# Performance work log

Hardware: AMD Instinct MI355X
Metric: run time of the kernel (lower is better)

Reference implementation:

```python
import jax, jax.numpy as jnp
import numpy as np

N_NODES = 100000
N_EDGES = 1600000
F_IN = 65
HIDDEN = 128
N_CLASSES = 32
NEG_SLOPE = 0.2


def _gat_conv(x0, src, dst, W, a_src, a_dst, b):
    """Single-head GAT-style conv: gather over edges, segment softmax, scatter-add."""
    h = x0 @ W                                  # [N, C]
    s = h @ a_src                                # [N]
    d = h @ a_dst                                # [N]
    e = jax.nn.leaky_relu(s[src] + d[dst], NEG_SLOPE)   # [E]
    m = jax.ops.segment_max(e, dst, num_segments=N_NODES)
    m = jnp.where(jnp.isfinite(m), m, 0.0)
    ex = jnp.exp(e - m[dst])                     # [E]
    denom = jax.ops.segment_sum(ex, dst, num_segments=N_NODES)
    alpha = ex / (denom[dst] + 1e-16)            # [E]
    out = jax.ops.segment_sum(h[src] * alpha[:, None], dst, num_segments=N_NODES)
    return out + b                               # [N, C]


def setup_inputs() -> dict:
    key = jax.random.key(0)
    ks = jax.random.split(key, 12)
    sc_in = 1.0 / np.sqrt(F_IN)
    sc_h = 1.0 / np.sqrt(HIDDEN)
    return {
        "x": jax.random.normal(ks[0], (N_NODES, F_IN), dtype=jnp.float32),
        "edge_index": jax.random.randint(ks[1], (2, N_EDGES), 0, N_NODES, dtype=jnp.int64),
        "W_mlp": jax.random.normal(ks[2], (F_IN, HIDDEN), dtype=jnp.float32) * sc_in,
        "b_mlp": jnp.zeros((HIDDEN,), dtype=jnp.float32),
        "W1": jax.random.normal(ks[3], (HIDDEN, N_CLASSES), dtype=jnp.float32) * sc_h,
        "a1_src": jax.random.normal(ks[4], (N_CLASSES,), dtype=jnp.float32) * 0.1,
        "a1_dst": jax.random.normal(ks[5], (N_CLASSES,), dtype=jnp.float32) * 0.1,
        "b1": jnp.zeros((N_CLASSES,), dtype=jnp.float32),
        "W2": jax.random.normal(ks[6], (HIDDEN, N_CLASSES), dtype=jnp.float32) * sc_h,
        "a2_src": jax.random.normal(ks[7], (N_CLASSES,), dtype=jnp.float32) * 0.1,
        "a2_dst": jax.random.normal(ks[8], (N_CLASSES,), dtype=jnp.float32) * 0.1,
        "b2": jnp.zeros((N_CLASSES,), dtype=jnp.float32),
    }


def reference(x, edge_index, W_mlp, b_mlp, W1, a1_src, a1_dst, b1, W2, a2_src, a2_dst, b2):
    src, dst = edge_index[0], edge_index[1]
    x0 = jax.nn.relu(x @ W_mlp + b_mlp)                      # [N, H]
    x1 = jax.nn.relu(_gat_conv(x0, src, dst, W1, a1_src, a1_dst, b1))  # [N, C]
    # dropout is identity in eval mode
    x2 = _gat_conv(x0, src, dst, W2, a2_src, a2_dst, b2)     # [N, C]
    x3 = jnp.max(x0, axis=-1, keepdims=True)                 # [N, 1]
    lngal_out = jnp.concatenate((x1, x2, x3), axis=-1) + x   # [N, 2C+1] == [N, F]
    return jax.nn.log_softmax(lngal_out, axis=1)
```

## Files before the change

kernel.cpp:

```cpp
#include <hip/hip_runtime.h>
#include <hip/hip_bf16.h>

#define NN 100000
#define NE 1600000
#define FIN 65
#define HID 128
#define NC 32
#define OUTC 65
#define NBUCK 391
#define CHUNKS 400
#define CH 4000
#define ESTRIDE 5120
#define NODE_BLOCKS 1563

typedef __attribute__((ext_vector_type(8))) short s8v;
typedef __attribute__((ext_vector_type(4))) float f4v;
typedef __attribute__((ext_vector_type(2))) float f2v;
#define MFMA16(a, b, c) __builtin_amdgcn_mfma_f32_16x16x32_bf16(a, b, c, 0, 0, 0)

__device__ __forceinline__ float lrelu(float v){ return v > 0.f ? v : 0.2f * v; }
__device__ __forceinline__ short f2bs(float f){
  unsigned u = __float_as_uint(f);
  u += 0x7fffu + ((u >> 16) & 1u);
  return (short)(u >> 16);
}
__device__ __forceinline__ float bfu_lo(unsigned u){ return __uint_as_float(u << 16); }
__device__ __forceinline__ float bfu_hi(unsigned u){ return __uint_as_float(u & 0xffff0000u); }
__device__ __forceinline__ unsigned char f2fp8(float f){
  int p = __builtin_amdgcn_cvt_pk_fp8_f32(f, f, 0, false);
  return (unsigned char)(p & 0xff);
}

__global__ __launch_bounds__(256) void k_prep(
    const float* __restrict__ Wmlp, const float* __restrict__ W1,
    const float* __restrict__ W2, short* __restrict__ wbg,
    int* __restrict__ bcursor)
{
  const int i = blockIdx.x * 256 + threadIdx.x;
  if (blockIdx.x == 0)
    for (int t = threadIdx.x; t < NBUCK; t += 256) bcursor[t] = 0;
  {
    const int j = i & 7, l = (i >> 3) & 63, nt = (i >> 9) & 7, t = i >> 12;
    const int k = t * 32 + ((l >> 4) << 3) + j;
    const int col = (nt << 4) + (l & 15);
    wbg[i] = f2bs(Wmlp[k * HID + col]);
  }
  {
    const int j = i & 7, l = (i >> 3) & 63, nt = (i >> 9) & 3, t = i >> 11;
    const int k = t * 32 + ((l >> 4) << 3) + j;
    const int col = (nt << 4) + (l & 15);
    wbg[8192 + i] = f2bs(col < NC ? W1[k * NC + col] : W2[k * NC + col - NC]);
  }
}

__global__ __launch_bounds__(256) void k_main(
    const float* __restrict__ x, const short* __restrict__ wbg,
    const float* __restrict__ Wmlp, const float* __restrict__ bmlp,
    const float* __restrict__ a1s, const float* __restrict__ a1d,
    const float* __restrict__ a2s, const float* __restrict__ a2d,
    const int* __restrict__ ei,
    unsigned char* __restrict__ hb8,
    float* __restrict__ sd2, float* __restrict__ dd2,
    float* __restrict__ out,
    int* __restrict__ bcursor, int* __restrict__ ebuf)
{
  __shared__ alignas(16) char smem[18944];
  const int tid = threadIdx.x;

  if (blockIdx.x >= NODE_BLOCKS) {
    const int cb = blockIdx.x - NODE_BLOCKS;
    int* lh = (int*)smem;
    int* lbase = lh + NBUCK;
    for (int i = tid; i < NBUCK; i += 256) lh[i] = 0;
    __syncthreads();
    const int4* s4 = (const int4*)ei + cb * (CH / 4);
    const int4* d4 = (const int4*)(ei + NE) + cb * (CH / 4);
    for (int i = tid; i < CH / 4; i += 256) {
      int4 v = d4[i];
      atomicAdd(&lh[v.x >> 8], 1);
      atomicAdd(&lh[v.y >> 8], 1);
      atomicAdd(&lh[v.z >> 8], 1);
      atomicAdd(&lh[v.w >> 8], 1);
    }
    __syncthreads();
    for (int i = tid; i < NBUCK; i += 256) {
      int c = lh[i];
      lbase[i] = c ? (i * ESTRIDE + atomicAdd(&bcursor[i], c)) : 0;
      lh[i] = 0;
    }
    __syncthreads();
    for (int i = tid; i < CH / 4; i += 256) {
      int4 sv = s4[i];
      int4 dv = d4[i];
      int b, r;
      b = dv.x >> 8; r = atomicAdd(&lh[b], 1); ebuf[lbase[b] + r] = (sv.x << 8) | (dv.x & 255);
      b = dv.y >> 8; r = atomicAdd(&lh[b], 1); ebuf[lbase[b] + r] = (sv.y << 8) | (dv.y & 255);
      b = dv.z >> 8; r = atomicAdd(&lh[b], 1); ebuf[lbase[b] + r] = (sv.z << 8) | (dv.z & 255);
      b = dv.w >> 8; r = atomicAdd(&lh[b], 1); ebuf[lbase[b] + r] = (sv.w << 8) | (dv.w & 255);
    }
    return;
  }

  short* x0b = (short*)smem;
  float* w64 = (float*)(smem + 17408);
  float* bmv = (float*)(smem + 17920);
  float* avv = (float*)(smem + 18432);

  const int base = blockIdx.x * 64;
  const int w = tid >> 6, lane = tid & 63;
  const int g = lane >> 4, q = lane & 15;
  const int rowA = w * 16 + q;
  const int rowD0 = w * 16 + g * 4;
  const int nodeA = base + rowA;
  const s8v* wv8 = (const s8v*)wbg;

  float xa[16];
  if (nodeA < NN) {
    const float* xr = x + (size_t)nodeA * FIN + g * 8;
    #pragma unroll
    for (int j = 0; j < 8; ++j) xa[j] = xr[j];
    #pragma unroll
    for (int j = 0; j < 8; ++j) xa[8 + j] = xr[32 + j];
  } else {
    #pragma unroll
    for (int j = 0; j < 16; ++j) xa[j] = 0.f;
  }
  float xc[4];
  #pragma unroll
  for (int r = 0; r < 4; ++r) {
    const int n2 = base + rowD0 + r;
    xc[r] = (n2 < NN) ? x[(size_t)n2 * FIN + 64] : 0.f;
  }

  if (tid < 128) { w64[tid] = Wmlp[64 * HID + tid]; bmv[tid] = bmlp[tid]; }
  else if (tid < 160) {
    const int qq = tid - 128;
    avv[qq] = a1s[qq]; avv[32 + qq] = a1d[qq]; avv[64 + qq] = a2s[qq]; avv[96 + qq] = a2d[qq];
  }
  __syncthreads();

  s8v a0, a1;
  #pragma unroll
  for (int j = 0; j < 8; ++j) { a0[j] = f2bs(xa[j]); a1[j] = f2bs(xa[8 + j]); }

  f4v acc[8];
  #pragma unroll
  for (int nt = 0; nt < 8; ++nt) acc[nt] = (f4v){0.f, 0.f, 0.f, 0.f};
  #pragma unroll
  for (int nt = 0; nt < 8; ++nt) {
    const s8v b0 = wv8[nt * 64 + lane];
    const s8v b1 = wv8[(8 + nt) * 64 + lane];
    acc[nt] = MFMA16(a0, b0, acc[nt]);
    acc[nt] = MFMA16(a1, b1, acc[nt]);
  }

  float rmax[4] = {0.f, 0.f, 0.f, 0.f};
  #pragma unroll
  for (int nt = 0; nt < 8; ++nt) {
    const int col = nt * 16 + q;
    const float wvv = w64[col], bv = bmv[col];
    #pragma unroll
    for (int r = 0; r < 4; ++r) {
      const float v = fmaxf(fmaf(xc[r], wvv, acc[nt][r]) + bv, 0.f);
      rmax[r] = fmaxf(rmax[r], v);
      x0b[(rowD0 + r) * 136 + col] = f2bs(v);
    }
  }
  #pragma unroll
  for (int off = 1; off < 16; off <<= 1)
    #pragma unroll
    for (int r = 0; r < 4; ++r) rmax[r] = fmaxf(rmax[r], __shfl_xor(rmax[r], off));
  if (q == 0) {
    #pragma unroll
    for (int r = 0; r < 4; ++r) {
      const int node = base + rowD0 + r;
      if (node < NN) out[(size_t)node * OUTC + 64] = rmax[r];
    }
  }

  s8v af[4];
  #pragma unroll
  for (int t2 = 0; t2 < 4; ++t2)
    af[t2] = *(const s8v*)&x0b[rowA * 136 + t2 * 32 + g * 8];
  f4v hacc[4];
  #pragma unroll
  for (int nt = 0; nt < 4; ++nt) hacc[nt] = (f4v){0.f, 0.f, 0.f, 0.f};
  #pragma unroll
  for (int nt = 0; nt < 4; ++nt)
    #pragma unroll
    for (int t2 = 0; t2 < 4; ++t2)
      hacc[nt] = MFMA16(af[t2], wv8[1024 + (t2 * 4 + nt) * 64 + lane], hacc[nt]);

  float s1p[4], d1p[4], s2p[4], d2p[4];
  #pragma unroll
  for (int r = 0; r < 4; ++r) {
    s1p[r] = hacc[0][r] * avv[q]        + hacc[1][r] * avv[16 + q];
    d1p[r] = hacc[0][r] * avv[32 + q]   + hacc[1][r] * avv[48 + q];
    s2p[r] = hacc[2][r] * avv[64 + q]   + hacc[3][r] * avv[80 + q];
    d2p[r] = hacc[2][r] * avv[96 + q]   + hacc[3][r] * avv[112 + q];
  }
  #pragma unroll
  for (int off = 1; off < 16; off <<= 1) {
    #pragma unroll
    for (int r = 0; r < 4; ++r) {
      s1p[r] += __shfl_xor(s1p[r], off);
      d1p[r] += __shfl_xor(d1p[r], off);
      s2p[r] += __shfl_xor(s2p[r], off);
      d2p[r] += __shfl_xor(d2p[r], off);
    }
  }
  #pragma unroll
  for (int r = 0; r < 4; ++r) {
    const int node = base + rowD0 + r;
    if (node < NN) {
      #pragma unroll
      for (int nt = 0; nt < 4; ++nt)
        hb8[(size_t)node * 64 + nt * 16 + q] = f2fp8(hacc[nt][r]);
      if (q == 0) {
        *(float2*)&sd2[(size_t)node * 2] = make_float2(s1p[r], s2p[r]);
        *(float2*)&dd2[(size_t)node * 2] = make_float2(d1p[r], d2p[r]);
      }
    }
  }
}

__global__ __launch_bounds__(256) void k_csr(const int* __restrict__ bcursor,
                                             const int* __restrict__ ebuf,
                                             int* __restrict__ rpp,
                                             int* __restrict__ csrc)
{
  __shared__ int lh[256];
  __shared__ int wsum[4];
  const int b = blockIdx.x;
  const int e0 = b * ESTRIDE;
  const int cntb = bcursor[b];
  const int t = threadIdx.x;

  lh[t] = 0;
  __syncthreads();
  for (int i = t; i < cntb; i += 256)
    atomicAdd(&lh[ebuf[e0 + i] & 255], 1);
  __syncthreads();

  const int lane = t & 63;
  const int wid = t >> 6;
  int v = lh[t];
  const int orig = v;
  for (int off = 1; off < 64; off <<= 1) {
    int tm = __shfl_up(v, off);
    if (lane >= off) v += tm;
  }
  if (lane == 63) wsum[wid] = v;
  __syncthreads();
  int add = 0;
  for (int ww = 0; ww < wid; ++ww) add += wsum[ww];
  const int ex = v + add - orig;

  const int nb0 = b << 8;
  if (nb0 + t < NN) rpp[nb0 + t] = ((e0 + ex) << 8) | orig;
  __syncthreads();
  lh[t] = ex;
  __syncthreads();
  for (int i = t; i < cntb; i += 256) {
    int p = ebuf[e0 + i];
    int r = atomicAdd(&lh[p & 255], 1);
    csrc[e0 + r] = ((unsigned)p) >> 8;
  }
}

__global__ __launch_bounds__(256) void k_conv(
    const int* __restrict__ rpp, const int* __restrict__ csrc,
    const unsigned char* __restrict__ hb8,
    const float* __restrict__ sd2, const float* __restrict__ dd2,
    const float* __restrict__ x,
    const float* __restrict__ b1, const float* __restrict__ b2,
    float* __restrict__ out)
{
  const int wid = threadIdx.x >> 6;
  const int lane = threadIdx.x & 63;
  const int half = lane >> 5;
  const int hl = lane & 31;
  const int eg = hl >> 4;
  const int cg = hl & 15;
  const int conv = cg >> 3;

  const int node = blockIdx.x * 8 + wid * 2 + half;

  const int rv = rpp[node];
  const int base = ((unsigned)rv) >> 8;
  const int cnt = rv & 255;
  const float2 dnv = *(const float2*)&dd2[(size_t)node * 2];

  float a0 = 0.f, a1 = 0.f, a2 = 0.f, a3 = 0.f;
  float den = 0.f;

  for (int chunk = 0; chunk < cnt; chunk += 32) {
    const int rem = min(cnt - chunk, 32);

    int sE = 0;
    float w1v = 0.f, w2v = 0.f;
    if (hl < rem) {
      sE = csrc[base + chunk + hl];
      const float2 sv = *(const float2*)&sd2[(size_t)sE * 2];
      w1v = __expf(lrelu(sv.x + dnv.x));
      w2v = __expf(lrelu(sv.y + dnv.y));
    }
    float d1 = w1v, d2 = w2v;
    #pragma unroll
    for (int off = 1; off < 32; off <<= 1) {
      d1 += __shfl_xor(d1, off);
      d2 += __shfl_xor(d2, off);
    }
    den += conv ? d2 : d1;

    const int wpk = (int)((((unsigned)(unsigned short)f2bs(w2v)) << 16) |
                           (unsigned)(unsigned short)f2bs(w1v));

    for (int i0 = 0; i0 < rem; i0 += 8) {
      #pragma unroll
      for (int u = 0; u < 4; ++u) {
        const int i = i0 + u * 2 + eg;
        const int src = half * 32 + i;
        const int s = __shfl(sE, src);
        const unsigned wp = (unsigned)__shfl(wpk, src);
        const float w = conv ? bfu_hi(wp) : bfu_lo(wp);
        const unsigned pv = *(const unsigned*)(hb8 + ((size_t)s << 6) + cg * 4);
        const f2v lo = __builtin_amdgcn_cvt_pk_f32_fp8((int)pv, false);
        const f2v hi = __builtin_amdgcn_cvt_pk_f32_fp8((int)pv, true);
        a0 = fmaf(w, lo[0], a0);
        a1 = fmaf(w, lo[1], a1);
        a2 = fmaf(w, hi[0], a2);
        a3 = fmaf(w, hi[1], a3);
      }
    }
  }

  a0 += __shfl_xor(a0, 16);
  a1 += __shfl_xor(a1, 16);
  a2 += __shfl_xor(a2, 16);
  a3 += __shfl_xor(a3, 16);

  const int ch = cg * 4;
  const float rden = 1.f / (den + 1e-16f);
  float v0 = a0 * rden, v1 = a1 * rden, v2 = a2 * rden, v3 = a3 * rden;
  if (conv == 0) {
    const float4 bv = *(const float4*)&b1[ch];
    v0 = fmaxf(v0 + bv.x, 0.f);
    v1 = fmaxf(v1 + bv.y, 0.f);
    v2 = fmaxf(v2 + bv.z, 0.f);
    v3 = fmaxf(v3 + bv.w, 0.f);
  } else {
    const float4 bv = *(const float4*)&b2[ch - 32];
    v0 += bv.x; v1 += bv.y; v2 += bv.z; v3 += bv.w;
  }
  const float* xr = x + (size_t)node * OUTC;
  float* row = out + (size_t)node * OUTC;
  const float4 xr4 = *(const float4*)&xr[ch];
  v0 += xr4.x; v1 += xr4.y; v2 += xr4.z; v3 += xr4.w;
  const float v64 = row[64] + xr[64];

  float mx = fmaxf(fmaxf(v0, v1), fmaxf(v2, v3));
  #pragma unroll
  for (int off = 1; off < 16; off <<= 1) mx = fmaxf(mx, __shfl_xor(mx, off));
  mx = fmaxf(mx, v64);
  float sm = __expf(v0 - mx) + __expf(v1 - mx) + __expf(v2 - mx) + __expf(v3 - mx);
  #pragma unroll
  for (int off = 1; off < 16; off <<= 1) sm += __shfl_xor(sm, off);
  sm += __expf(v64 - mx);
  const float ls = __logf(sm);

  if (eg == 0) {
    *(float4*)&row[ch] = make_float4(v0 - mx - ls, v1 - mx - ls, v2 - mx - ls, v3 - mx - ls);
    if (hl == 0) row[64] = v64 - mx - ls;
  }
}

extern "C" void kernel_launch(void* const* d_in, const int* in_sizes, int n_in,
                              void* d_out, int out_size, void* d_ws, size_t ws_size,
                              hipStream_t stream)
{
  const float* x    = (const float*)d_in[0];
  const int*   ei   = (const int*)d_in[1];
  const float* Wmlp = (const float*)d_in[2];
  const float* bmlp = (const float*)d_in[3];
  const float* W1   = (const float*)d_in[4];
  const float* a1s  = (const float*)d_in[5];
  const float* a1d  = (const float*)d_in[6];
  const float* b1   = (const float*)d_in[7];
  const float* W2   = (const float*)d_in[8];
  const float* a2s  = (const float*)d_in[9];
  const float* a2d  = (const float*)d_in[10];
  const float* b2   = (const float*)d_in[11];
  float* out = (float*)d_out;

  unsigned char* hb8 = (unsigned char*)d_ws;
  float* sd2 = (float*)(hb8 + (size_t)NN * 64);
  float* dd2 = sd2 + (size_t)2 * NN;
  int* ebuf   = (int*)(dd2 + (size_t)2 * NN);
  int* csrc   = ebuf + (size_t)NBUCK * ESTRIDE;
  int* rpp    = csrc + (size_t)NBUCK * ESTRIDE;
  int* bcursor= rpp + NBUCK * 256;
  short* wbg  = (short*)(bcursor + NBUCK);

  k_prep<<<32, 256, 0, stream>>>(Wmlp, W1, W2, wbg, bcursor);

  k_main<<<NODE_BLOCKS + CHUNKS, 256, 0, stream>>>(
      x, wbg, Wmlp, bmlp, a1s, a1d, a2s, a2d, ei,
      hb8, sd2, dd2, out, bcursor, ebuf);

  k_csr<<<NBUCK, 256, 0, stream>>>(bcursor, ebuf, rpp, csrc);

  k_conv<<<NN / 8, 256, 0, stream>>>(rpp, csrc, hb8, sd2, dd2, x, b1, b2, out);
}
```

Baseline: 95.68 us.

## Split GAT conv into two passes over separate half-width fp8 feature arrays

The fp8 hidden features are now written as two separate 32-byte-per-node arrays, one per conv. The single aggregation kernel becomes two templated passes, each gathering only its own half. The intent is to shrink the random-gather working set per pass so it fits better in cache, and to drop the bf16 weight packing. The cost is reading the CSR and source scores twice, an extra kernel launch, and a round trip of the first conv's output through global memory before the second pass applies log-softmax. Non-temporal loads and stores are also added.

```diff
diff --git a/kernel.cpp b/kernel.cpp
--- a/kernel.cpp
+++ b/kernel.cpp
@@ -59,7 +59,7 @@
     const float* __restrict__ a1s, const float* __restrict__ a1d,
     const float* __restrict__ a2s, const float* __restrict__ a2d,
     const int* __restrict__ ei,
-    unsigned char* __restrict__ hb8,
+    unsigned char* __restrict__ hb8a, unsigned char* __restrict__ hb8b,
     float* __restrict__ sd2, float* __restrict__ dd2,
     float* __restrict__ out,
     int* __restrict__ bcursor, int* __restrict__ ebuf)
@@ -214,8 +214,10 @@
     const int node = base + rowD0 + r;
     if (node < NN) {
       #pragma unroll
-      for (int nt = 0; nt < 4; ++nt)
-        hb8[(size_t)node * 64 + nt * 16 + q] = f2fp8(hacc[nt][r]);
+      for (int nt = 0; nt < 4; ++nt) {
+        unsigned char* hp = (nt < 2) ? hb8a : hb8b;
+        hp[(size_t)node * 32 + (nt & 1) * 16 + q] = f2fp8(hacc[nt][r]);
+      }
       if (q == 0) {
         *(float2*)&sd2[(size_t)node * 2] = make_float2(s1p[r], s2p[r]);
         *(float2*)&dd2[(size_t)node * 2] = make_float2(d1p[r], d2p[r]);
@@ -268,112 +270,121 @@
   }
 }
 
+template<int P>
 __global__ __launch_bounds__(256) void k_conv(
     const int* __restrict__ rpp, const int* __restrict__ csrc,
-    const unsigned char* __restrict__ hb8,
+    const unsigned char* __restrict__ hbP,
     const float* __restrict__ sd2, const float* __restrict__ dd2,
     const float* __restrict__ x,
-    const float* __restrict__ b1, const float* __restrict__ b2,
+    const float* __restrict__ bias,
     float* __restrict__ out)
 {
   const int wid = threadIdx.x >> 6;
   const int lane = threadIdx.x & 63;
   const int half = lane >> 5;
   const int hl = lane & 31;
-  const int eg = hl >> 4;
-  const int cg = hl & 15;
-  const int conv = cg >> 3;
+  const int sub = hl >> 3;
+  const int c8 = hl & 7;
 
   const int node = blockIdx.x * 8 + wid * 2 + half;
 
   const int rv = rpp[node];
   const int base = ((unsigned)rv) >> 8;
   const int cnt = rv & 255;
-  const float2 dnv = *(const float2*)&dd2[(size_t)node * 2];
-
-  float a0 = 0.f, a1 = 0.f, a2 = 0.f, a3 = 0.f;
-  float den = 0.f;
+  const float dn = dd2[(size_t)node * 2 + P];
+
+  float a[4] = {0.f, 0.f, 0.f, 0.f};
+  float dsum = 0.f;
 
   for (int chunk = 0; chunk < cnt; chunk += 32) {
     const int rem = min(cnt - chunk, 32);
 
     int sE = 0;
-    float w1v = 0.f, w2v = 0.f;
+    float wE = 0.f;
     if (hl < rem) {
-      sE = csrc[base + chunk + hl];
-      const float2 sv = *(const float2*)&sd2[(size_t)sE * 2];
-      w1v = __expf(lrelu(sv.x + dnv.x));
-      w2v = __expf(lrelu(sv.y + dnv.y));
-    }
-    float d1 = w1v, d2 = w2v;
-    #pragma unroll
-    for (int off = 1; off < 32; off <<= 1) {
-      d1 += __shfl_xor(d1, off);
-      d2 += __shfl_xor(d2, off);
-    }
-    den += conv ? d2 : d1;
-
-    const int wpk = (int)((((unsigned)(unsigned short)f2bs(w2v)) << 16) |
-                           (unsigned)(unsigned short)f2bs(w1v));
-
-    for (int i0 = 0; i0 < rem; i0 += 8) {
+      sE = __builtin_nontemporal_load(&csrc[base + chunk + hl]);
+      const float sv = sd2[(size_t)sE * 2 + P];
+      wE = __expf(lrelu(sv + dn));
+    }
+
+    for (int i0 = 0; i0 < rem; i0 += 4) {
+      const int i = i0 + sub;
+      const int srcl = half * 32 + i;
+      const int s = __shfl(sE, srcl);
+      const float wgt = __shfl(wE, srcl);
+      dsum += wgt;
+      const unsigned pv = *(const unsigned*)(hbP + ((size_t)s << 5) + c8 * 4);
+      const f2v lo = __builtin_amdgcn_cvt_pk_f32_fp8((int)pv, false);
+      const f2v hi = __builtin_amdgcn_cvt_pk_f32_fp8((int)pv, true);
+      a[0] = fmaf(wgt, lo[0], a[0]);
+      a[1] = fmaf(wgt, lo[1], a[1]);
+      a[2] = fmaf(wgt, hi[0], a[2]);
+      a[3] = fmaf(wgt, hi[1], a[3]);
+    }
+  }
+
+  #pragma unroll
+  for (int j = 0; j < 4; ++j) {
+    a[j] += __shfl_xor(a[j], 8);
+    a[j] += __shfl_xor(a[j], 16);
+  }
+  dsum += __shfl_xor(dsum, 8);
+  dsum += __shfl_xor(dsum, 16);
+
+  const float rden = 1.f / (dsum + 1e-16f);
+  const int ch = c8 * 4;
+  const float* xr = x + (size_t)node * OUTC + P * 32;
+  float v[4];
+  #pragma unroll
+  for (int j = 0; j < 4; ++j) {
+    float t = fmaf(a[j], rden, bias[ch + j]);
+    if (P == 0) t = fmaxf(t, 0.f);
+    v[j] = t + __builtin_nontemporal_load(&xr[ch + j]);
+  }
+
+  float* row = out + (size_t)node * OUTC;
+  if (P == 0) {
+    if (sub == 0) {
       #pragma unroll
-      for (int u = 0; u < 4; ++u) {
-        const int i = i0 + u * 2 + eg;
-        const int src = half * 32 + i;
-        const int s = __shfl(sE, src);
-        const unsigned wp = (unsigned)__shfl(wpk, src);
-        const float w = conv ? bfu_hi(wp) : bfu_lo(wp);
-        const unsigned pv = *(const unsigned*)(hb8 + ((size_t)s << 6) + cg * 4);
-        const f2v lo = __builtin_amdgcn_cvt_pk_f32_fp8((int)pv, false);
-        const f2v hi = __builtin_amdgcn_cvt_pk_f32_fp8((int)pv, true);
-        a0 = fmaf(w, lo[0], a0);
-        a1 = fmaf(w, lo[1], a1);
-        a2 = fmaf(w, hi[0], a2);
-        a3 = fmaf(w, hi[1], a3);
+      for (int j = 0; j < 4; ++j)
+        __builtin_nontemporal_store(v[j], &row[ch + j]);
+    }
+  } else {
+    float r0[4];
+    #pragma unroll
+    for (int j = 0; j < 4; ++j) r0[j] = row[ch + j];
+    const float v64 = row[64] + __builtin_nontemporal_load(&x[(size_t)node * OUTC + 64]);
+
+    float mx = v64;
+    #pragma unroll
+    for (int j = 0; j < 4; ++j) mx = fmaxf(mx, fmaxf(v[j], r0[j]));
+    #pragma unroll
+    for (int off = 1; off < 8; off <<= 1) mx = fmaxf(mx, __shfl_xor(mx, off));
+    float sm = 0.f;
+    #pragma unroll
+    for (int j = 0; j < 4; ++j) sm += __expf(v[j] - mx) + __expf(r0[j] - mx);
+    #pragma unroll
+    for (int off = 1; off < 8; off <<= 1) sm += __shfl_xor(sm, off);
+    sm += __expf(v64 - mx);
+    const float ls = __logf(sm) + mx;
+
+    if (sub == 0) {
+      #pragma unroll
+      for (int j = 0; j < 4; ++j) {
+        __builtin_nontemporal_store(r0[j] - ls, &row[ch + j]);
+        __builtin_nontemporal_store(v[j] - ls, &row[32 + ch + j]);
       }
-    }
-  }
-
-  a0 += __shfl_xor(a0, 16);
-  a1 += __shfl_xor(a1, 16);
-  a2 += __shfl_xor(a2, 16);
-  a3 += __shfl_xor(a3, 16);
-
-  const int ch = cg * 4;
-  const float rden = 1.f / (den + 1e-16f);
-  float v0 = a0 * rden, v1 = a1 * rden, v2 = a2 * rden, v3 = a3 * rden;
-  if (conv == 0) {
-    const float4 bv = *(const float4*)&b1[ch];
-    v0 = fmaxf(v0 + bv.x, 0.f);
-    v1 = fmaxf(v1 + bv.y, 0.f);
-    v2 = fmaxf(v2 + bv.z, 0.f);
-    v3 = fmaxf(v3 + bv.w, 0.f);
-  } else {
-    const float4 bv = *(const float4*)&b2[ch - 32];
-    v0 += bv.x; v1 += bv.y; v2 += bv.z; v3 += bv.w;
-  }
-  const float* xr = x + (size_t)node * OUTC;
-  float* row = out + (size_t)node * OUTC;
-  const float4 xr4 = *(const float4*)&xr[ch];
-  v0 += xr4.x; v1 += xr4.y; v2 += xr4.z; v3 += xr4.w;
-  const float v64 = row[64] + xr[64];
-
-  float mx = fmaxf(fmaxf(v0, v1), fmaxf(v2, v3));
-  #pragma unroll
-  for (int off = 1; off < 16; off <<= 1) mx = fmaxf(mx, __shfl_xor(mx, off));
-  mx = fmaxf(mx, v64);
-  float sm = __expf(v0 - mx) + __expf(v1 - mx) + __expf(v2 - mx) + __expf(v3 - mx);
-  #pragma unroll
-  for (int off = 1; off < 16; off <<= 1) sm += __shfl_xor(sm, off);
-  sm += __expf(v64 - mx);
-  const float ls = __logf(sm);
-
-  if (eg == 0) {
-    *(float4*)&row[ch] = make_float4(v0 - mx - ls, v1 - mx - ls, v2 - mx - ls, v3 - mx - ls);
-    if (hl == 0) row[64] = v64 - mx - ls;
-  }
-}
+      if (hl == 0) __builtin_nontemporal_store(v64 - ls, &row[64]);
+    }
+  }
+}
+
+template __global__ void k_conv<0>(const int*, const int*, const unsigned char*,
+                                   const float*, const float*, const float*,
+                                   const float*, float*);
+template __global__ void k_conv<1>(const int*, const int*, const unsigned char*,
+                                   const float*, const float*, const float*,
+                                   const float*, float*);
 
 extern "C" void kernel_launch(void* const* d_in, const int* in_sizes, int n_in,
                               void* d_out, int out_size, void* d_ws, size_t ws_size,
@@ -393,8 +404,9 @@
   const float* b2   = (const float*)d_in[11];
   float* out = (float*)d_out;
 
-  unsigned char* hb8 = (unsigned char*)d_ws;
-  float* sd2 = (float*)(hb8 + (size_t)NN * 64);
+  unsigned char* hb8a = (unsigned char*)d_ws;
+  unsigned char* hb8b = hb8a + (size_t)NN * 32;
+  float* sd2 = (float*)(hb8b + (size_t)NN * 32);
   float* dd2 = sd2 + (size_t)2 * NN;
   int* ebuf   = (int*)(dd2 + (size_t)2 * NN);
   int* csrc   = ebuf + (size_t)NBUCK * ESTRIDE;
@@ -406,9 +418,10 @@
 
   k_main<<<NODE_BLOCKS + CHUNKS, 256, 0, stream>>>(
       x, wbg, Wmlp, bmlp, a1s, a1d, a2s, a2d, ei,
-      hb8, sd2, dd2, out, bcursor, ebuf);
+      hb8a, hb8b, sd2, dd2, out, bcursor, ebuf);
 
   k_csr<<<NBUCK, 256, 0, stream>>>(bcursor, ebuf, rpp, csrc);
 
-  k_conv<<<NN / 8, 256, 0, stream>>>(rpp, csrc, hb8, sd2, dd2, x, b1, b2, out);
-}
+  k_conv<0><<<NN / 8, 256, 0, stream>>>(rpp, csrc, hb8a, sd2, dd2, x, b1, out);
+  k_conv<1><<<NN / 8, 256, 0, stream>>>(rpp, csrc, hb8b, sd2, dd2, x, b2, out);
+}
```

Result: slower. 134.5 us (+40.6%).
